# Kernel tuning notes

Hardware: AMD Instinct MI355X
Metric: run time of the kernel (lower is better)

## Reference

```python
import jax, jax.numpy as jnp
import numpy as np

B = 16384       # batch
G = 8           # groups
S = 16          # state_c (per-group in/out channels)
H = 512         # hidden_c (per-group hidden channels)
FACTOR = 1.0
SWISH_DIV = 1.1


def setup_inputs() -> dict:
    key = jax.random.key(0)
    ks = jax.random.split(key, 12)
    def w(k, shape, fan_in):
        bound = 1.0 / np.sqrt(fan_in)
        return jax.random.uniform(k, shape, jnp.float32, -bound, bound)
    return {
        "x":  jax.random.normal(ks[0], (B, G * S), dtype=jnp.float32),
        # grouped 1x1 convs as per-group linear weights [G, out_c, in_c]
        "W1": w(ks[1], (G, H, S), S), "b1": w(ks[2], (G, H), S),
        "beta1": jnp.full((G,), 0.5, jnp.float32),
        "W2": w(ks[3], (G, H, H), H), "b2": w(ks[4], (G, H), H),
        "beta2": jnp.full((G,), 0.5, jnp.float32),
        "W3": w(ks[5], (G, H, H), H), "b3": w(ks[6], (G, H), H),
        "beta3": jnp.full((G,), 0.5, jnp.float32),
        "W4": w(ks[7], (G, S, H), H), "b4": w(ks[8], (G, S), H),
    }


def _group_swish(x, beta):
    # x: [B, G, C]; beta: [G] -> y = x * sigmoid(x * softplus(beta)) / 1.1
    sp = jax.nn.softplus(beta)[None, :, None]
    return x * jax.nn.sigmoid(x * sp) / SWISH_DIV


def reference(x, W1, b1, beta1, W2, b2, beta2, W3, b3, beta3, W4, b4):
    h = x.reshape(-1, G, S)                                   # [B,G,S]
    h = jnp.einsum('bgs,ghs->bgh', h, W1) + b1[None]          # [B,G,H]
    h = _group_swish(h, beta1)
    h = jnp.einsum('bgi,goi->bgo', h, W2) + b2[None]
    h = _group_swish(h, beta2)
    h = jnp.einsum('bgi,goi->bgo', h, W3) + b3[None]
    h = _group_swish(h, beta3)
    h = jnp.einsum('bgh,gsh->bgs', h, W4) + b4[None]          # [B,G,S]
    return h.reshape(-1, G * S) * FACTOR
```

## Files before the change

### kernel.cpp

```cpp
#include <hip/hip_runtime.h>
#include <stdint.h>

#define G_ 8
#define S_ 16
#define H_ 512
#define TB 64
#define NTH 256

typedef _Float16 h16;
typedef _Float16 h16x8 __attribute__((ext_vector_type(8)));
typedef float f32x4 __attribute__((ext_vector_type(4)));
typedef float f32x16 __attribute__((ext_vector_type(16)));

#define HB_BYTES (TB * 1024)
#define XB_BYTES 2048
#define SMEM_BYTES (HB_BYTES + XB_BYTES)


__device__ __forceinline__ float swishf(float v, float sp) {
    const float e = __expf(-v * sp);
    return v * __builtin_amdgcn_rcpf(1.0f + e) * (1.0f / 1.1f);
}

__device__ __forceinline__ uint32_t pk16(float a, float b) {
    return __builtin_bit_cast(uint32_t, __builtin_amdgcn_cvt_pkrtz(a, b));
}

template<bool USEWS>
__device__ __forceinline__ h16x8 loadA32ks(const h16* __restrict__ wpk,
                                           const float* __restrict__ wf,
                                           int ks, int nb, int ln, int Ksrc) {
    if constexpr (USEWS) {
        return *(const h16x8*)(wpk + (((size_t)ks * 16 + nb) * 64 + ln) * 8);
    } else {
        const int row = nb * 32 + (ln & 31);
        const int k = ks * 16 + (ln >> 5) * 8;
        const float* p = wf + (size_t)row * Ksrc + k;
        h16x8 r;
        #pragma unroll
        for (int j = 0; j < 8; ++j) r[j] = (h16)p[j];
        return r;
    }
}

template<bool USEWS>
__device__ __forceinline__ h16x8 loadA16(const h16* __restrict__ wpk,
                                         const float* __restrict__ wf,
                                         int ks32, int ln, int Ksrc) {
    if constexpr (USEWS) {
        return *(const h16x8*)(wpk + ((size_t)ks32 * 64 + ln) * 8);
    } else {
        const int row = ln & 15;
        const int k = ks32 * 32 + (ln >> 4) * 8;
        const float* p = wf + (size_t)row * Ksrc + k;
        h16x8 r;
        #pragma unroll
        for (int j = 0; j < 8; ++j) r[j] = (h16)p[j];
        return r;
    }
}

__device__ __forceinline__ void swish_store32(const f32x16 (&acc)[4][2], char* hb,
                                              const float* __restrict__ bias, float sp,
                                              int wv, int ln) {
    const int l31 = ln & 31, lh = ln >> 5;
    char* const wbase = hb + wv * 16384 + l31 * 16 + lh * 8;
    #pragma unroll
    for (int ot = 0; ot < 4; ++ot) {
        #pragma unroll
        for (int rq = 0; rq < 4; ++rq) {
            const int col0 = wv * 128 + ot * 32 + rq * 8 + lh * 4;
            const f32x4 bv = *(const f32x4*)(bias + col0);
            #pragma unroll
            for (int bt = 0; bt < 2; ++bt) {
                const float v0 = swishf(acc[ot][bt][rq * 4 + 0] + bv[0], sp);
                const float v1 = swishf(acc[ot][bt][rq * 4 + 1] + bv[1], sp);
                const float v2 = swishf(acc[ot][bt][rq * 4 + 2] + bv[2], sp);
                const float v3 = swishf(acc[ot][bt][rq * 4 + 3] + bv[3], sp);
                const uint64_t u = (uint64_t)pk16(v0, v1)
                                 | ((uint64_t)pk16(v2, v3) << 32);
                *(uint64_t*)(wbase + (ot * 4 + rq) * 1024 + bt * 512) = u;
            }
        }
    }
}

template<bool USEWS>
__device__ __forceinline__ void layerH32(f32x16 (&acc)[4][2],
                                         const h16* __restrict__ wpk, const float* __restrict__ wf,
                                         const char* __restrict__ hb, int wv, int ln) {
    const int l31 = ln & 31, lh = ln >> 5;
    const char* const bbase = hb + l31 * 16 + lh * 1024;
    const int nb0 = wv * 4;
    #pragma unroll
    for (int ot = 0; ot < 4; ++ot)
        #pragma unroll
        for (int bt = 0; bt < 2; ++bt) acc[ot][bt] = (f32x16)(0.f);

    #pragma unroll 2
    for (int ks = 0; ks < 32; ++ks) {
        h16x8 a[4];
        #pragma unroll
        for (int ot = 0; ot < 4; ++ot)
            a[ot] = loadA32ks<USEWS>(wpk, wf, ks, nb0 + ot, ln, H_);
        const h16x8 b0 = *(const h16x8*)(bbase + ks * 2048);
        const h16x8 b1 = *(const h16x8*)(bbase + ks * 2048 + 512);
        __builtin_amdgcn_s_setprio(1);
        #pragma unroll
        for (int ot = 0; ot < 4; ++ot) {
            acc[ot][0] = __builtin_amdgcn_mfma_f32_32x32x16_f16(a[ot], b0, acc[ot][0], 0, 0, 0);
            acc[ot][1] = __builtin_amdgcn_mfma_f32_32x32x16_f16(a[ot], b1, acc[ot][1], 0, 0, 0);
        }
        __builtin_amdgcn_s_setprio(0);
    }
}

template<bool USEWS>
__global__ __launch_bounds__(NTH, 2) void mlp_fused(
    const float* __restrict__ x,
    const float* __restrict__ W1f, const float* __restrict__ b1, const float* __restrict__ be1,
    const float* __restrict__ W2f, const float* __restrict__ b2, const float* __restrict__ be2,
    const float* __restrict__ W3f, const float* __restrict__ b3, const float* __restrict__ be3,
    const float* __restrict__ W4f, const float* __restrict__ b4,
    const h16* __restrict__ W1p, const h16* __restrict__ W2p,
    const h16* __restrict__ W3p, const h16* __restrict__ W4p,
    float* __restrict__ out) {
    extern __shared__ char smem[];
    char* __restrict__ xb = smem + HB_BYTES;

    const int bid = blockIdx.x;
    const int g = bid & 7;
    const int rowbase = (bid >> 3) * TB;
    const int tid = threadIdx.x;
    const int wv = tid >> 6;
    const int ln = tid & 63;
    const int l31 = ln & 31;
    const int lh = ln >> 5;

    const float sp1 = log1pf(__expf(be1[g]));
    const float sp2 = log1pf(__expf(be2[g]));
    const float sp3 = log1pf(__expf(be3[g]));

    const h16* w1p = W1p + (size_t)g * H_ * S_;
    const h16* w2p = W2p + (size_t)g * H_ * H_;
    const h16* w3p = W3p + (size_t)g * H_ * H_;
    const h16* w4p = W4p + (size_t)g * S_ * H_;
    const float* w1f = W1f + (size_t)g * H_ * S_;
    const float* w2f = W2f + (size_t)g * H_ * H_;
    const float* w3f = W3f + (size_t)g * H_ * H_;
    const float* w4f = W4f + (size_t)g * S_ * H_;

    {
        const int idx = tid * 4;
        const int r = idx >> 4, s = idx & 15;
        const f32x4 v = *(const f32x4*)(x + (size_t)(rowbase + r) * (G_ * S_) + g * S_ + s);
        const uint64_t u = (uint64_t)pk16(v[0], v[1]) | ((uint64_t)pk16(v[2], v[3]) << 32);
        *(uint64_t*)(xb + (s >> 3) * 1024 + r * 16 + (s & 7) * 2) = u;
    }
    __syncthreads();

    f32x16 acc[4][2];

    {
        #pragma unroll
        for (int ot = 0; ot < 4; ++ot)
            #pragma unroll
            for (int bt = 0; bt < 2; ++bt) acc[ot][bt] = (f32x16)(0.f);
        const char* const xbase = xb + l31 * 16 + lh * 1024;
        const h16x8 bX0 = *(const h16x8*)(xbase);
        const h16x8 bX1 = *(const h16x8*)(xbase + 512);
        #pragma unroll
        for (int ot = 0; ot < 4; ++ot) {
            const h16x8 aW = loadA32ks<USEWS>(w1p, w1f, 0, wv * 4 + ot, ln, S_);
            acc[ot][0] = __builtin_amdgcn_mfma_f32_32x32x16_f16(aW, bX0, acc[ot][0], 0, 0, 0);
            acc[ot][1] = __builtin_amdgcn_mfma_f32_32x32x16_f16(aW, bX1, acc[ot][1], 0, 0, 0);
        }
    }
    swish_store32(acc, smem, b1 + g * H_, sp1, wv, ln);
    __syncthreads();

    layerH32<USEWS>(acc, w2p, w2f, smem, wv, ln);
    __syncthreads();
    swish_store32(acc, smem, b2 + g * H_, sp2, wv, ln);
    __syncthreads();

    layerH32<USEWS>(acc, w3p, w3f, smem, wv, ln);
    __syncthreads();
    swish_store32(acc, smem, b3 + g * H_, sp3, wv, ln);
    __syncthreads();

    {
        f32x4 a4 = {0.f, 0.f, 0.f, 0.f};
        const int l15 = ln & 15, lq = ln >> 4;
        const char* const b4base = smem + lq * 1024 + (wv * 16 + l15) * 16;
        #pragma unroll 4
        for (int ks = 0; ks < 16; ++ks) {
            const h16x8 a = loadA16<USEWS>(w4p, w4f, ks, ln, H_);
            const h16x8 b = *(const h16x8*)(b4base + ks * 4096);
            a4 = __builtin_amdgcn_mfma_f32_16x16x32_f16(a, b, a4, 0, 0, 0);
        }
        const int brow = wv * 16 + l15;
        const int s0 = lq * 4;
        const f32x4 bv = *(const f32x4*)(b4 + g * S_ + s0);
        f32x4 o4;
        #pragma unroll
        for (int r = 0; r < 4; ++r) o4[r] = a4[r] + bv[r];
        *(f32x4*)(out + (size_t)(rowbase + brow) * (G_ * S_) + g * S_ + s0) = o4;
    }
}

__global__ void packW32(const float* __restrict__ s, h16* __restrict__ d,
                        int KB, int Ks) {
    const int t = blockIdx.x * 256 + threadIdx.x;
    const int total = G_ * KB * 16 * 64;
    if (t >= total) return;
    const int ln = t & 63;
    const int blk = t >> 6;
    const int nb = blk & 15;
    const int rest = blk >> 4;
    const int ks = rest % KB;
    const int g = rest / KB;
    const int row = g * H_ + nb * 32 + (ln & 31);
    const int k = ks * 16 + (ln >> 5) * 8;
    const float* p = s + (size_t)row * Ks + k;
    h16x8 o;
    #pragma unroll
    for (int j = 0; j < 8; ++j) o[j] = (h16)p[j];
    *(h16x8*)(d + (size_t)t * 8) = o;
}

__global__ void packW16(const float* __restrict__ s, h16* __restrict__ d,
                        int NB_total, int KB, int Ks) {
    const int t = blockIdx.x * 256 + threadIdx.x;
    const int total = NB_total * KB * 64;
    if (t >= total) return;
    const int ln = t & 63;
    const int blk = t >> 6;
    const int kb = blk % KB;
    const int nbg = blk / KB;
    const int row = nbg * 16 + (ln & 15);
    const int k = kb * 32 + (ln >> 4) * 8;
    const float* p = s + (size_t)row * Ks + k;
    h16x8 o;
    #pragma unroll
    for (int j = 0; j < 8; ++j) o[j] = (h16)p[j];
    *(h16x8*)(d + (size_t)t * 8) = o;
}

extern "C" void kernel_launch(void* const* d_in, const int* in_sizes, int n_in,
                              void* d_out, int out_size, void* d_ws, size_t ws_size,
                              hipStream_t stream) {
    const float* x   = (const float*)d_in[0];
    const float* W1  = (const float*)d_in[1];
    const float* b1  = (const float*)d_in[2];
    const float* be1 = (const float*)d_in[3];
    const float* W2  = (const float*)d_in[4];
    const float* b2  = (const float*)d_in[5];
    const float* be2 = (const float*)d_in[6];
    const float* W3  = (const float*)d_in[7];
    const float* b3  = (const float*)d_in[8];
    const float* be3 = (const float*)d_in[9];
    const float* W4  = (const float*)d_in[10];
    const float* b4  = (const float*)d_in[11];
    float* out = (float*)d_out;

    const size_t nW2  = (size_t)G_ * H_ * H_;
    const size_t nW1p = (size_t)G_ * H_ * S_;
    const size_t nW4  = (size_t)G_ * S_ * H_;
    const size_t need = (2 * nW2 + nW1p + nW4) * sizeof(h16);

    const dim3 grid((16384 / TB) * G_), blk(NTH);

    if (ws_size >= need) {
        h16* W2p = (h16*)d_ws;
        h16* W3p = W2p + nW2;
        h16* W1p = W3p + nW2;
        h16* W4p = W1p + nW1p;
        packW32<<<dim3((unsigned)((nW2 / 8 + 255) / 256)), dim3(256), 0, stream>>>(W2, W2p, 32, H_);
        packW32<<<dim3((unsigned)((nW2 / 8 + 255) / 256)), dim3(256), 0, stream>>>(W3, W3p, 32, H_);
        packW32<<<dim3((unsigned)((nW1p / 8 + 255) / 256)), dim3(256), 0, stream>>>(W1, W1p, 1, S_);
        packW16<<<dim3((unsigned)((nW4 / 8 + 255) / 256)), dim3(256), 0, stream>>>(W4, W4p, G_, 16, H_);
        (void)hipFuncSetAttribute(reinterpret_cast<const void*>(mlp_fused<true>),
                                  hipFuncAttributeMaxDynamicSharedMemorySize, (int)SMEM_BYTES);
        mlp_fused<true><<<grid, blk, SMEM_BYTES, stream>>>(
            x, W1, b1, be1, W2, b2, be2, W3, b3, be3, W4, b4,
            W1p, W2p, W3p, W4p, out);
    } else {
        (void)hipFuncSetAttribute(reinterpret_cast<const void*>(mlp_fused<false>),
                                  hipFuncAttributeMaxDynamicSharedMemorySize, (int)SMEM_BYTES);
        mlp_fused<false><<<grid, blk, SMEM_BYTES, stream>>>(
            x, W1, b1, be1, W2, b2, be2, W3, b3, be3, W4, b4,
            nullptr, nullptr, nullptr, nullptr, out);
    }
}
```

Measured before the change: 191.1 us.

## Replace block barriers with per-wave LDS flag handoff between MLP layers

Replaces the __syncthreads barriers between hidden layers with per-wave LDS counters: each wave reads the hidden buffer in quarter-sized chunks, starting at its own quarter and rotating, and signals when it has finished reading each chunk. A wave then overwrites its own quarter once all four readers are done. This lets waves start the next layer on chunks that are already ready instead of waiting for the whole block. In exchange it adds spin-wait polling with s_sleep and hand-written fences, which carries memory-ordering risk and polling overhead.

Result: slower. 197.9 us (+3.5%).

```diff
diff --git a/kernel.cpp b/kernel.cpp
--- a/kernel.cpp
+++ b/kernel.cpp
@@ -14,8 +14,18 @@
 
 #define HB_BYTES (TB * 1024)
 #define XB_BYTES 2048
-#define SMEM_BYTES (HB_BYTES + XB_BYTES)
-
+#define FLAG_BYTES 64
+#define SMEM_BYTES (HB_BYTES + XB_BYTES + FLAG_BYTES)
+
+
+__device__ __forceinline__ void fence_acquire() {
+    __builtin_amdgcn_sched_barrier(0);
+    asm volatile("" ::: "memory");
+}
+__device__ __forceinline__ void fence_release() {
+    asm volatile("s_waitcnt lgkmcnt(0)" ::: "memory");
+    __builtin_amdgcn_sched_barrier(0);
+}
 
 __device__ __forceinline__ float swishf(float v, float sp) {
     const float e = __expf(-v * sp);
@@ -60,9 +70,16 @@
     }
 }
 
+template<bool FLAGS>
 __device__ __forceinline__ void swish_store32(const f32x16 (&acc)[4][2], char* hb,
                                               const float* __restrict__ bias, float sp,
-                                              int wv, int ln) {
+                                              int wv, int ln,
+                                              int* rdone, volatile int* wdone,
+                                              int need, int wseq) {
+    if constexpr (FLAGS) {
+        while (*(volatile int*)&rdone[wv] < need) __builtin_amdgcn_s_sleep(1);
+        fence_acquire();
+    }
     const int l31 = ln & 31, lh = ln >> 5;
     char* const wbase = hb + wv * 16384 + l31 * 16 + lh * 8;
     #pragma unroll
@@ -83,12 +100,17 @@
             }
         }
     }
-}
-
-template<bool USEWS>
+    if constexpr (FLAGS) {
+        fence_release();
+        if (ln == 0) *(volatile int*)&wdone[wv] = wseq;
+    }
+}
+
+template<bool USEWS, bool POLLW>
 __device__ __forceinline__ void layerH32(f32x16 (&acc)[4][2],
                                          const h16* __restrict__ wpk, const float* __restrict__ wf,
-                                         const char* __restrict__ hb, int wv, int ln) {
+                                         const char* __restrict__ hb, int wv, int ln,
+                                         volatile int* wdone, int* rdone, int wseq) {
     const int l31 = ln & 31, lh = ln >> 5;
     const char* const bbase = hb + l31 * 16 + lh * 1024;
     const int nb0 = wv * 4;
@@ -97,21 +119,32 @@
         #pragma unroll
         for (int bt = 0; bt < 2; ++bt) acc[ot][bt] = (f32x16)(0.f);
 
-    #pragma unroll 2
-    for (int ks = 0; ks < 32; ++ks) {
-        h16x8 a[4];
-        #pragma unroll
-        for (int ot = 0; ot < 4; ++ot)
-            a[ot] = loadA32ks<USEWS>(wpk, wf, ks, nb0 + ot, ln, H_);
-        const h16x8 b0 = *(const h16x8*)(bbase + ks * 2048);
-        const h16x8 b1 = *(const h16x8*)(bbase + ks * 2048 + 512);
-        __builtin_amdgcn_s_setprio(1);
-        #pragma unroll
-        for (int ot = 0; ot < 4; ++ot) {
-            acc[ot][0] = __builtin_amdgcn_mfma_f32_32x32x16_f16(a[ot], b0, acc[ot][0], 0, 0, 0);
-            acc[ot][1] = __builtin_amdgcn_mfma_f32_32x32x16_f16(a[ot], b1, acc[ot][1], 0, 0, 0);
-        }
-        __builtin_amdgcn_s_setprio(0);
+    for (int i = 0; i < 4; ++i) {
+        const int q = (wv + i) & 3;
+        if constexpr (POLLW) {
+            while (wdone[q] < wseq) __builtin_amdgcn_s_sleep(1);
+            fence_acquire();
+        }
+        const char* const qb = bbase + q * 16384;
+        #pragma unroll 4
+        for (int j = 0; j < 8; ++j) {
+            const int ks = q * 8 + j;
+            h16x8 a[4];
+            #pragma unroll
+            for (int ot = 0; ot < 4; ++ot)
+                a[ot] = loadA32ks<USEWS>(wpk, wf, ks, nb0 + ot, ln, H_);
+            const h16x8 b0 = *(const h16x8*)(qb + j * 2048);
+            const h16x8 b1 = *(const h16x8*)(qb + j * 2048 + 512);
+            __builtin_amdgcn_s_setprio(1);
+            #pragma unroll
+            for (int ot = 0; ot < 4; ++ot) {
+                acc[ot][0] = __builtin_amdgcn_mfma_f32_32x32x16_f16(a[ot], b0, acc[ot][0], 0, 0, 0);
+                acc[ot][1] = __builtin_amdgcn_mfma_f32_32x32x16_f16(a[ot], b1, acc[ot][1], 0, 0, 0);
+            }
+            __builtin_amdgcn_s_setprio(0);
+        }
+        fence_release();
+        if (ln == 0) atomicAdd(&rdone[q], 1);
     }
 }
 
@@ -127,6 +160,9 @@
     float* __restrict__ out) {
     extern __shared__ char smem[];
     char* __restrict__ xb = smem + HB_BYTES;
+    int* const flagbase = (int*)(smem + HB_BYTES + XB_BYTES);
+    volatile int* const wdone = (volatile int*)flagbase;
+    int* const rdone = flagbase + 4;
 
     const int bid = blockIdx.x;
     const int g = bid & 7;
@@ -150,6 +186,7 @@
     const float* w3f = W3f + (size_t)g * H_ * H_;
     const float* w4f = W4f + (size_t)g * S_ * H_;
 
+    if (tid < 8) flagbase[tid] = 0;
     {
         const int idx = tid * 4;
         const int r = idx >> 4, s = idx & 15;
@@ -176,28 +213,30 @@
             acc[ot][1] = __builtin_amdgcn_mfma_f32_32x32x16_f16(aW, bX1, acc[ot][1], 0, 0, 0);
         }
     }
-    swish_store32(acc, smem, b1 + g * H_, sp1, wv, ln);
+    swish_store32<false>(acc, smem, b1 + g * H_, sp1, wv, ln, nullptr, nullptr, 0, 0);
     __syncthreads();
 
-    layerH32<USEWS>(acc, w2p, w2f, smem, wv, ln);
-    __syncthreads();
-    swish_store32(acc, smem, b2 + g * H_, sp2, wv, ln);
-    __syncthreads();
-
-    layerH32<USEWS>(acc, w3p, w3f, smem, wv, ln);
-    __syncthreads();
-    swish_store32(acc, smem, b3 + g * H_, sp3, wv, ln);
-    __syncthreads();
+    layerH32<USEWS, false>(acc, w2p, w2f, smem, wv, ln, wdone, rdone, 0);
+    swish_store32<true>(acc, smem, b2 + g * H_, sp2, wv, ln, rdone, wdone, 4, 2);
+
+    layerH32<USEWS, true>(acc, w3p, w3f, smem, wv, ln, wdone, rdone, 2);
+    swish_store32<true>(acc, smem, b3 + g * H_, sp3, wv, ln, rdone, wdone, 8, 3);
 
     {
         f32x4 a4 = {0.f, 0.f, 0.f, 0.f};
         const int l15 = ln & 15, lq = ln >> 4;
         const char* const b4base = smem + lq * 1024 + (wv * 16 + l15) * 16;
-        #pragma unroll 4
-        for (int ks = 0; ks < 16; ++ks) {
-            const h16x8 a = loadA16<USEWS>(w4p, w4f, ks, ln, H_);
-            const h16x8 b = *(const h16x8*)(b4base + ks * 4096);
-            a4 = __builtin_amdgcn_mfma_f32_16x16x32_f16(a, b, a4, 0, 0, 0);
+        for (int i = 0; i < 4; ++i) {
+            const int q = (wv + i) & 3;
+            while (wdone[q] < 3) __builtin_amdgcn_s_sleep(1);
+            fence_acquire();
+            #pragma unroll
+            for (int j = 0; j < 4; ++j) {
+                const int ks = q * 4 + j;
+                const h16x8 a = loadA16<USEWS>(w4p, w4f, ks, ln, H_);
+                const h16x8 b = *(const h16x8*)(b4base + ks * 4096);
+                a4 = __builtin_amdgcn_mfma_f32_16x16x32_f16(a, b, a4, 0, 0, 0);
+            }
         }
         const int brow = wv * 16 + l15;
         const int s0 = lq * 4;
```
